# Kernel tuning notes

Measured on AMD Instinct MI355X. Metric: run time of the kernel, lower is better.

The kernel has to match this reference:

```python
import jax, jax.numpy as jnp
import numpy as np

N, E, C, S, G = 20000, 320000, 32, 64, 64
NRAD, HRAD, OUTS, HHEAD, NSH, NL = 8, 64, 16, 64, 9, 2
RCUT = 5.0
LIDX = np.repeat(np.arange(3), [1, 3, 5])  # l index of each of the 9 sh components


def _sph_harm(u):
    # real spherical harmonics up to l=2 on unit vectors, [E,3] -> [E,9]
    x, y, z = u[:, 0], u[:, 1], u[:, 2]
    s3 = jnp.sqrt(jnp.asarray(3.0, u.dtype))
    return jnp.stack([
        jnp.ones_like(x), x, y, z,
        s3 * x * y, s3 * y * z, 0.5 * (3 * z * z - 1.0), s3 * x * z,
        0.5 * s3 * (x * x - y * y)
    ], axis=1)


def _bessel(r):
    # Bessel radial basis with smooth polynomial envelope, [E] -> [E, NRAD]
    n = jnp.arange(1, NRAD + 1, dtype=r.dtype)
    rs = jnp.clip(r, 1e-6, None)[:, None]
    u = jnp.clip(r / RCUT, 0.0, 1.0)
    env = ((1 - u) ** 2 * (1 + 2 * u))[:, None]
    return jnp.sqrt(2.0 / RCUT) * jnp.sin(n * jnp.pi * rs / RCUT) / rs * env


def setup_inputs() -> dict:
    key = jax.random.key(0)
    ks = jax.random.split(key, 16)
    return {
        'vectors': jax.random.normal(ks[0], (E, 3), jnp.float32),
        'node_species': jax.random.randint(ks[1], (N,), 0, S),
        'senders': jax.random.randint(ks[2], (E,), 0, N),
        'receivers': jax.random.randint(ks[3], (E,), 0, N),
        'graph_id': jnp.sort(jax.random.randint(ks[4], (N,), 0, G)),
        'species_embed': jax.random.normal(ks[5], (S, C), jnp.float32) * 0.1,
        'w_r1': jax.random.normal(ks[6], (NRAD, HRAD), jnp.float32) / np.sqrt(NRAD),
        'b_r1': jnp.zeros((HRAD,), jnp.float32),
        'w_r2': jax.random.normal(ks[7], (NL, HRAD, 3 * C), jnp.float32) / np.sqrt(HRAD),
        'w_mix': jax.random.normal(ks[8], (NL, 3, C, C), jnp.float32) / np.sqrt(C),
        'w_sc': jax.random.normal(ks[9], (NL, S, C, C), jnp.float32) / np.sqrt(C),
        'w_readout': jax.random.normal(ks[10], (C, OUTS), jnp.float32) / np.sqrt(C),
        'ln_gamma': jnp.ones((OUTS,), jnp.float32),
        'ln_beta': jnp.zeros((OUTS,), jnp.float32),
        'w_h1': jax.random.normal(ks[11], (OUTS, HHEAD), jnp.float32) / np.sqrt(OUTS),
        'b_h1': jnp.zeros((HHEAD,), jnp.float32),
        'w_h2': jax.random.normal(ks[12], (HHEAD, 1), jnp.float32) / np.sqrt(HHEAD),
        'b_h2': jnp.zeros((1,), jnp.float32),
        'scale': jnp.ones((), jnp.float32),
        'shift': jnp.zeros((), jnp.float32),
    }


def reference(vectors, node_species, senders, receivers, graph_id, species_embed,
              w_r1, b_r1, w_r2, w_mix, w_sc, w_readout, ln_gamma, ln_beta,
              w_h1, b_h1, w_h2, b_h2, scale, shift):
    lidx = jnp.asarray(LIDX)
    # nan-safe edge norms and unit vectors (safe_norm in source)
    r2 = jnp.sum(vectors ** 2, axis=-1)
    r = jnp.where(r2 == 0, 0.0, jnp.sqrt(jnp.where(r2 == 0, 1.0, r2)))
    u = vectors / jnp.where(r == 0, 1.0, r)[:, None]
    sh = _sph_harm(u)                                  # [E,9]
    rad = jax.nn.silu(_bessel(r) @ w_r1 + b_r1)        # [E,HRAD] radial MLP
    h = species_embed[node_species]                    # [N,C] node embedding
    for li in range(NL):
        # per-edge, per-l, per-channel radial weights, expanded to the 9 sh components
        rw = (rad @ w_r2[li]).reshape(E, 3, C)[:, lidx, :]     # [E,9,C]
        # tensor-product message: radial * sender scalars * Y_lm
        msg = sh[:, :, None] * rw * h[senders][:, None, :]     # [E,9,C]
        agg = jax.ops.segment_sum(msg, receivers, num_segments=N)  # [N,9,C]
        # per-irrep (per-l) channel-mixing linear
        mixed = jnp.einsum('nmc,mcd->nmd', agg, w_mix[li][lidx])   # [N,9,C]
        # species-dependent self-connection on the scalar (l=0) channel
        sc = jnp.einsum('nc,ncd->nd', h, w_sc[li][node_species])   # [N,C]
        h = mixed[:, 0, :] + sc + h                                # residual
    readout = h @ w_readout                            # [N,OUTS] (last-block readout)
    mu = jnp.mean(readout, axis=-1, keepdims=True)
    var = jnp.var(readout, axis=-1, keepdims=True)
    nrm = (readout - mu) * jax.lax.rsqrt(var + 1e-6) * ln_gamma + ln_beta
    node_out = (jax.nn.gelu(nrm @ w_h1 + b_h1) @ w_h2 + b_h2)[:, 0]  # [N]
    gsum = jax.ops.segment_sum(node_out, graph_id, num_segments=G)
    cnt = jax.ops.segment_sum(jnp.ones((N,), node_out.dtype), graph_id, num_segments=G)
    gmean = gsum / jnp.clip(cnt, 1.0, None)            # segment-mean node2graph
    return (gmean * scale + shift)[:, None]            # [G,1]
```

## Files before the change

kernel.cpp:

```cpp
#include <hip/hip_runtime.h>
#include <hip/hip_fp16.h>
#include <cstdint>
#include <cmath>

#define NE 320000
#define NN 20000
#define NG 64

typedef __attribute__((ext_vector_type(8))) short s16x8;
typedef __attribute__((ext_vector_type(4))) float f32x4;

static __device__ __forceinline__ unsigned short f32_to_bf16(float x) {
    unsigned int u = __float_as_uint(x);
    u = (u + 0x7fffu + ((u >> 16) & 1u)) >> 16;
    return (unsigned short)u;
}
static __device__ __forceinline__ float bf16_to_f32(unsigned short h) {
    return __uint_as_float(((unsigned int)h) << 16);
}

__global__ __launch_bounds__(256) void setup_kernel(
    const int* __restrict__ spec, const float* __restrict__ emb,
    float* __restrict__ h,
    const float* __restrict__ w_r2,
    unsigned short* __restrict__ wt_hi, unsigned short* __restrict__ wt_lo,
    int* __restrict__ deg, float* __restrict__ gz)
{
    int t = blockIdx.x * 256 + threadIdx.x;
    if (t < NN * 32) h[t] = emb[spec[t >> 5] * 32 + (t & 31)];
    if (t < 4096) {
        int c = t >> 6, k = t & 63;
        float v = w_r2[(c >= 32 ? 6144 : 0) + k * 96 + (c & 31)];
        unsigned short hb = f32_to_bf16(v);
        wt_hi[t] = hb;
        wt_lo[t] = f32_to_bf16(v - bf16_to_f32(hb));
    }
    if (t < NN) deg[t] = 0;
    if (t < 128) gz[t] = 0.0f;
}

__global__ __launch_bounds__(256) void count_kernel(
    const int* __restrict__ recv, int* __restrict__ deg)
{
    int e = blockIdx.x * 256 + threadIdx.x;
    atomicAdd(&deg[recv[e]], 1);
}

__global__ __launch_bounds__(1024) void scan_kernel(
    const int* __restrict__ deg,
    int* __restrict__ rowstart, int* __restrict__ cursor)
{
    __shared__ int tsum[1024];
    const int tid = threadIdx.x;
    const int PER = (NN + 1023) / 1024;
    const int base = tid * PER;

    int s = 0;
    for (int i = 0; i < PER; ++i) {
        int idx = base + i;
        if (idx < NN) s += deg[idx];
    }
    tsum[tid] = s;
    __syncthreads();
    for (int off = 1; off < 1024; off <<= 1) {
        int v = (tid >= off) ? tsum[tid - off] : 0;
        __syncthreads();
        tsum[tid] += v;
        __syncthreads();
    }
    int run = tsum[tid] - s;
    for (int i = 0; i < PER; ++i) {
        int idx = base + i;
        if (idx < NN) {
            rowstart[idx] = run;
            cursor[idx] = run;
            run += deg[idx];
        }
    }
    if (tid == 1023) rowstart[NN] = NE;
}

__global__ __launch_bounds__(256) void scatter_kernel(
    const int* __restrict__ recv, const int* __restrict__ snd,
    int* __restrict__ cursor, int* __restrict__ eperm, int* __restrict__ esnd)
{
    int e = blockIdx.x * 256 + threadIdx.x;
    int slot = atomicAdd(&cursor[recv[e]], 1);
    eperm[e] = slot;
    esnd[slot] = snd[e];
}

__global__ __launch_bounds__(256) void edge_gemm_kernel(
    const float* __restrict__ vectors,
    const float* __restrict__ w_r1,
    const float* __restrict__ b_r1,
    const unsigned short* __restrict__ wt_hi,
    const unsigned short* __restrict__ wt_lo,
    const int* __restrict__ eperm,
    __half* __restrict__ rw0_0,
    __half* __restrict__ rw0_1)
{
    __shared__ __attribute__((aligned(16))) short sh_hi[256 * 72];
    __shared__ __attribute__((aligned(16))) short sh_lo[256 * 72];

    const int tid = threadIdx.x;
    const int e = blockIdx.x * 256 + tid;
    const int slot = eperm[e];

    float x = vectors[3 * e + 0];
    float y = vectors[3 * e + 1];
    float z = vectors[3 * e + 2];
    float r2 = x * x + y * y + z * z;
    float r = (r2 == 0.0f) ? 0.0f : sqrtf(r2);
    float rs = fmaxf(r, 1e-6f);
    float u = fminf(r * 0.2f, 1.0f);
    float env = (1.0f - u) * (1.0f - u) * (1.0f + 2.0f * u);
    float pref = 0.6324555320336759f * env / rs;
    float theta = 0.6283185307179586f * rs;

    float s1 = __sinf(theta), c1 = __cosf(theta);
    float twoc = 2.0f * c1;
    float b[8];
    {
        float sp = 0.0f, s = s1;
#pragma unroll
        for (int n = 0; n < 8; ++n) {
            b[n] = pref * s;
            float nx = twoc * s - sp;
            sp = s; s = nx;
        }
    }

#pragma unroll
    for (int j0 = 0; j0 < 64; j0 += 8) {
        short hibuf[8], lobuf[8];
#pragma unroll
        for (int jj = 0; jj < 8; ++jj) {
            int j = j0 + jj;
            float pre = b_r1[j];
#pragma unroll
            for (int n = 0; n < 8; ++n) pre = fmaf(b[n], w_r1[n * 64 + j], pre);
            float rj = pre * __builtin_amdgcn_rcpf(1.0f + __expf(-pre));
            unsigned short hb = f32_to_bf16(rj);
            float lov = rj - bf16_to_f32(hb);
            hibuf[jj] = (short)hb;
            lobuf[jj] = (short)f32_to_bf16(lov);
        }
        *(s16x8*)&sh_hi[tid * 72 + j0] =
            (s16x8){hibuf[0],hibuf[1],hibuf[2],hibuf[3],hibuf[4],hibuf[5],hibuf[6],hibuf[7]};
        *(s16x8*)&sh_lo[tid * 72 + j0] =
            (s16x8){lobuf[0],lobuf[1],lobuf[2],lobuf[3],lobuf[4],lobuf[5],lobuf[6],lobuf[7]};
    }

    __syncthreads();

    const int wv = tid >> 6;
    const int l = tid & 63;
    const int lrow = l & 15;
    const int lk = l >> 4;

    s16x8 Bhi[4][2], Blo[4][2];
#pragma unroll
    for (int ct = 0; ct < 4; ++ct)
#pragma unroll
        for (int kt = 0; kt < 2; ++kt) {
            int col = ct * 16 + lrow;
            int kof = kt * 32 + lk * 8;
            Bhi[ct][kt] = *(const s16x8*)(wt_hi + col * 64 + kof);
            Blo[ct][kt] = *(const s16x8*)(wt_lo + col * 64 + kof);
        }

    f32x4 acc[4][4];
#pragma unroll
    for (int rt = 0; rt < 4; ++rt)
#pragma unroll
        for (int ct = 0; ct < 4; ++ct) acc[rt][ct] = (f32x4){0.f, 0.f, 0.f, 0.f};

#pragma unroll
    for (int rt = 0; rt < 4; ++rt) {
        int row = wv * 64 + rt * 16 + lrow;
#pragma unroll
        for (int kt = 0; kt < 2; ++kt) {
            s16x8 ahi = *(const s16x8*)&sh_hi[row * 72 + kt * 32 + lk * 8];
            s16x8 alo = *(const s16x8*)&sh_lo[row * 72 + kt * 32 + lk * 8];
#pragma unroll
            for (int ct = 0; ct < 4; ++ct) {
                acc[rt][ct] = __builtin_amdgcn_mfma_f32_16x16x32_bf16(ahi, Bhi[ct][kt], acc[rt][ct], 0, 0, 0);
                acc[rt][ct] = __builtin_amdgcn_mfma_f32_16x16x32_bf16(alo, Bhi[ct][kt], acc[rt][ct], 0, 0, 0);
                acc[rt][ct] = __builtin_amdgcn_mfma_f32_16x16x32_bf16(ahi, Blo[ct][kt], acc[rt][ct], 0, 0, 0);
            }
        }
    }

    __syncthreads();
    __half* stg = (__half*)sh_hi;
#pragma unroll
    for (int rt = 0; rt < 4; ++rt)
#pragma unroll
        for (int ct = 0; ct < 4; ++ct) {
            int col = ct * 16 + lrow;
#pragma unroll
            for (int rr = 0; rr < 4; ++rr) {
                int erow = wv * 64 + rt * 16 + lk * 4 + rr;
                stg[erow * 72 + col] = __float2half_rn(acc[rt][ct][rr]);
            }
        }
    __syncthreads();
    {
        const s16x8* src = (const s16x8*)&sh_hi[tid * 72];
        size_t eb = (size_t)slot * 32;
        s16x8* d0 = (s16x8*)(rw0_0 + eb);
        s16x8* d1 = (s16x8*)(rw0_1 + eb);
        d0[0] = src[0]; d0[1] = src[1]; d0[2] = src[2]; d0[3] = src[3];
        d1[0] = src[4]; d1[1] = src[5]; d1[2] = src[6]; d1[3] = src[7];
    }
}

__device__ __forceinline__ float agg_update_val(
    const __half* __restrict__ rw0h, const float* __restrict__ hin,
    const int* __restrict__ rowstart, const int* __restrict__ esnd,
    const int* __restrict__ spec,
    const float* __restrict__ wmix0, const float* __restrict__ wscl,
    int t, int n, int c, int half)
{
    int s0 = rowstart[n], s1 = rowstart[n + 1];
    float hv = hin[t];

    float p0 = 0.f, p1 = 0.f, p2 = 0.f, p3 = 0.f;
    int k = s0;
    for (; k + 4 <= s1; k += 4) {
        int sA = esnd[k], sB = esnd[k + 1], sC = esnd[k + 2], sD = esnd[k + 3];
        float rA = __half2float(rw0h[(size_t)k * 32 + c]);
        float rB = __half2float(rw0h[(size_t)(k + 1) * 32 + c]);
        float rC = __half2float(rw0h[(size_t)(k + 2) * 32 + c]);
        float rD = __half2float(rw0h[(size_t)(k + 3) * 32 + c]);
        float hA = hin[(size_t)sA * 32 + c];
        float hB = hin[(size_t)sB * 32 + c];
        float hC = hin[(size_t)sC * 32 + c];
        float hD = hin[(size_t)sD * 32 + c];
        p0 = fmaf(rA, hA, p0);
        p1 = fmaf(rB, hB, p1);
        p2 = fmaf(rC, hC, p2);
        p3 = fmaf(rD, hD, p3);
    }
    for (; k < s1; ++k)
        p0 = fmaf(__half2float(rw0h[(size_t)k * 32 + c]),
                  hin[(size_t)esnd[k] * 32 + c], p0);
    float acc = (p0 + p1) + (p2 + p3);

    const float* wsc = wscl + spec[n] * 1024;
    float m0 = 0.f, m1 = 0.f, q0 = 0.f, q1 = 0.f;
#pragma unroll
    for (int cp = 0; cp < 32; cp += 2) {
        float av0 = __shfl(acc, half + cp);
        float hb0 = __shfl(hv, half + cp);
        float av1 = __shfl(acc, half + cp + 1);
        float hb1 = __shfl(hv, half + cp + 1);
        m0 = fmaf(av0, wmix0[cp * 32 + c], m0);
        q0 = fmaf(hb0, wsc[cp * 32 + c], q0);
        m1 = fmaf(av1, wmix0[(cp + 1) * 32 + c], m1);
        q1 = fmaf(hb1, wsc[(cp + 1) * 32 + c], q1);
    }
    return hv + (m0 + m1) + (q0 + q1);
}

__global__ __launch_bounds__(256) void agg_update_kernel(
    const __half* __restrict__ rw0h, const float* __restrict__ hin,
    const int* __restrict__ rowstart, const int* __restrict__ esnd,
    const int* __restrict__ spec,
    const float* __restrict__ wmix0, const float* __restrict__ wscl,
    float* __restrict__ hout)
{
    int t = blockIdx.x * 256 + threadIdx.x;
    int n = t >> 5, c = t & 31;
    int half = (threadIdx.x & 63) & 32;
    hout[t] = agg_update_val(rw0h, hin, rowstart, esnd, spec, wmix0, wscl,
                             t, n, c, half);
}

__global__ __launch_bounds__(256) void agg_readout_kernel(
    const __half* __restrict__ rw0h, const float* __restrict__ hin,
    const int* __restrict__ rowstart, const int* __restrict__ esnd,
    const int* __restrict__ spec,
    const float* __restrict__ wmix0, const float* __restrict__ wscl,
    const int* __restrict__ gid_arr,
    const float* __restrict__ w_ro,
    const float* __restrict__ gamma, const float* __restrict__ beta,
    const float* __restrict__ w_h1, const float* __restrict__ b_h1,
    const float* __restrict__ w_h2, const float* __restrict__ b_h2,
    float* __restrict__ gsum, float* __restrict__ gcnt)
{
    __shared__ int sgid[8];
    __shared__ float sval[8];

    int t = blockIdx.x * 256 + threadIdx.x;
    int n = t >> 5, c = t & 31;
    int half = (threadIdx.x & 63) & 32;

    float outv = agg_update_val(rw0h, hin, rowstart, esnd, spec, wmix0, wscl,
                                t, n, c, half);

    int o = c & 15;
    float r0 = 0.f, r1 = 0.f, r2 = 0.f, r3 = 0.f;
#pragma unroll
    for (int cp = 0; cp < 32; cp += 4) {
        r0 = fmaf(__shfl(outv, half + cp),     w_ro[cp * 16 + o],       r0);
        r1 = fmaf(__shfl(outv, half + cp + 1), w_ro[(cp + 1) * 16 + o], r1);
        r2 = fmaf(__shfl(outv, half + cp + 2), w_ro[(cp + 2) * 16 + o], r2);
        r3 = fmaf(__shfl(outv, half + cp + 3), w_ro[(cp + 3) * 16 + o], r3);
    }
    float ro = (r0 + r1) + (r2 + r3);

    float ssum = ro;
#pragma unroll
    for (int m = 1; m < 16; m <<= 1) ssum += __shfl_xor(ssum, m);
    float mu = ssum * (1.0f / 16.0f);
    float d = ro - mu;
    float vs = d * d;
#pragma unroll
    for (int m = 1; m < 16; m <<= 1) vs += __shfl_xor(vs, m);
    float inv = rsqrtf(vs * (1.0f / 16.0f) + 1e-6f);
    float nrm = d * inv * gamma[o] + beta[o];

    int j1 = c, j2 = c + 32;
    float a1a = b_h1[j1], a1b = 0.f, a2a = b_h1[j2], a2b = 0.f;
#pragma unroll
    for (int oo = 0; oo < 16; oo += 2) {
        float nv0 = __shfl(nrm, half + oo);
        float nv1 = __shfl(nrm, half + oo + 1);
        a1a = fmaf(nv0, w_h1[oo * 64 + j1], a1a);
        a2a = fmaf(nv0, w_h1[oo * 64 + j2], a2a);
        a1b = fmaf(nv1, w_h1[(oo + 1) * 64 + j1], a1b);
        a2b = fmaf(nv1, w_h1[(oo + 1) * 64 + j2], a2b);
    }
    float a1 = a1a + a1b, a2 = a2a + a2b;
    float g1 = 0.5f * a1 * (1.0f + tanhf(0.7978845608028654f * (a1 + 0.044715f * a1 * a1 * a1)));
    float g2 = 0.5f * a2 * (1.0f + tanhf(0.7978845608028654f * (a2 + 0.044715f * a2 * a2 * a2)));
    float partial = fmaf(g1, w_h2[j1], g2 * w_h2[j2]);
#pragma unroll
    for (int m = 1; m < 32; m <<= 1) partial += __shfl_xor(partial, m);

    if (c == 0) {
        int hw = threadIdx.x >> 5;
        sgid[hw] = gid_arr[n];
        sval[hw] = partial + b_h2[0];
    }
    __syncthreads();
    if (threadIdx.x == 0) {
        int g0 = sgid[0];
        float accv = sval[0];
        float cnt = 1.0f;
        for (int i = 1; i < 8; ++i) {
            if (sgid[i] == g0) { accv += sval[i]; cnt += 1.0f; }
            else {
                atomicAdd(&gsum[g0], accv);
                atomicAdd(&gcnt[g0], cnt);
                g0 = sgid[i]; accv = sval[i]; cnt = 1.0f;
            }
        }
        atomicAdd(&gsum[g0], accv);
        atomicAdd(&gcnt[g0], cnt);
    }
}

__global__ void finalize_kernel(const float* __restrict__ gsum,
                                const float* __restrict__ gcnt,
                                const float* __restrict__ scale,
                                const float* __restrict__ shift,
                                float* __restrict__ out)
{
    int g = threadIdx.x;
    if (g < NG) out[g] = gsum[g] / fmaxf(gcnt[g], 1.0f) * scale[0] + shift[0];
}

extern "C" void kernel_launch(void* const* d_in, const int* in_sizes, int n_in,
                              void* d_out, int out_size, void* d_ws, size_t ws_size,
                              hipStream_t stream)
{
    const float* vectors       = (const float*)d_in[0];
    const int*   node_species  = (const int*)d_in[1];
    const int*   senders       = (const int*)d_in[2];
    const int*   receivers     = (const int*)d_in[3];
    const int*   graph_id      = (const int*)d_in[4];
    const float* species_embed = (const float*)d_in[5];
    const float* w_r1          = (const float*)d_in[6];
    const float* b_r1          = (const float*)d_in[7];
    const float* w_r2          = (const float*)d_in[8];
    const float* w_mix         = (const float*)d_in[9];
    const float* w_sc          = (const float*)d_in[10];
    const float* w_ro          = (const float*)d_in[11];
    const float* ln_gamma      = (const float*)d_in[12];
    const float* ln_beta       = (const float*)d_in[13];
    const float* w_h1          = (const float*)d_in[14];
    const float* b_h1          = (const float*)d_in[15];
    const float* w_h2          = (const float*)d_in[16];
    const float* b_h2          = (const float*)d_in[17];
    const float* scale         = (const float*)d_in[18];
    const float* shift         = (const float*)d_in[19];
    float* out = (float*)d_out;

    __half* rw0_0 = (__half*)d_ws;
    __half* rw0_1 = rw0_0 + (size_t)NE * 32;
    float* hA     = (float*)(rw0_1 + (size_t)NE * 32);
    float* hB     = hA + (size_t)NN * 32;
    float* gsum   = hB + (size_t)NN * 32;
    float* gcnt   = gsum + NG;
    unsigned short* wt_hi = (unsigned short*)(gcnt + NG);
    unsigned short* wt_lo = wt_hi + 4096;
    int* deg      = (int*)(wt_lo + 4096);
    int* rowstart = deg + NN;
    int* cursor   = rowstart + NN + 1;
    int* eperm    = cursor + NN + 1;
    int* esnd     = eperm + NE;

    setup_kernel<<<(NN * 32 + 255) / 256, 256, 0, stream>>>(
        node_species, species_embed, hA, w_r2, wt_hi, wt_lo, deg, gsum);

    count_kernel<<<NE / 256, 256, 0, stream>>>(receivers, deg);

    scan_kernel<<<1, 1024, 0, stream>>>(deg, rowstart, cursor);

    scatter_kernel<<<NE / 256, 256, 0, stream>>>(receivers, senders, cursor, eperm, esnd);

    edge_gemm_kernel<<<NE / 256, 256, 0, stream>>>(
        vectors, w_r1, b_r1, wt_hi, wt_lo, eperm, rw0_0, rw0_1);

    agg_update_kernel<<<(NN * 32) / 256, 256, 0, stream>>>(
        rw0_0, hA, rowstart, esnd, node_species, w_mix, w_sc, hB);

    agg_readout_kernel<<<(NN * 32) / 256, 256, 0, stream>>>(
        rw0_1, hB, rowstart, esnd, node_species, w_mix + 3072, w_sc + 65536,
        graph_id, w_ro, ln_gamma, ln_beta, w_h1, b_h1, w_h2, b_h2, gsum, gcnt);

    finalize_kernel<<<1, 64, 0, stream>>>(gsum, gcnt, scale, shift, out);
}
```

Before: 174.7 us.

## Fuse CSR build stages, interleave radial weights, stage sender indices in LDS

```diff
diff --git a/kernel.cpp b/kernel.cpp
--- a/kernel.cpp
+++ b/kernel.cpp
@@ -21,13 +21,13 @@
 
 __global__ __launch_bounds__(256) void setup_kernel(
     const int* __restrict__ spec, const float* __restrict__ emb,
-    float* __restrict__ h,
+    float* __restrict__ hA,
     const float* __restrict__ w_r2,
     unsigned short* __restrict__ wt_hi, unsigned short* __restrict__ wt_lo,
-    int* __restrict__ deg, float* __restrict__ gz)
+    int* __restrict__ deg, float* __restrict__ gz, int* __restrict__ tickets)
 {
     int t = blockIdx.x * 256 + threadIdx.x;
-    if (t < NN * 32) h[t] = emb[spec[t >> 5] * 32 + (t & 31)];
+    if (t < NN * 32) hA[t] = emb[spec[t >> 5] * 32 + (t & 31)];
     if (t < 4096) {
         int c = t >> 6, k = t & 63;
         float v = w_r2[(c >= 32 ? 6144 : 0) + k * 96 + (c & 31)];
@@ -37,24 +37,27 @@
     }
     if (t < NN) deg[t] = 0;
     if (t < 128) gz[t] = 0.0f;
-}
-
-__global__ __launch_bounds__(256) void count_kernel(
-    const int* __restrict__ recv, int* __restrict__ deg)
-{
-    int e = blockIdx.x * 256 + threadIdx.x;
-    atomicAdd(&deg[recv[e]], 1);
-}
-
-__global__ __launch_bounds__(1024) void scan_kernel(
-    const int* __restrict__ deg,
-    int* __restrict__ rowstart, int* __restrict__ cursor)
-{
+    if (t < 2) tickets[t] = 0;
+}
+
+__global__ __launch_bounds__(1024) void count_scan_kernel(
+    const int* __restrict__ recv,
+    int* __restrict__ deg, int* __restrict__ rowstart, int* __restrict__ cursor,
+    int* __restrict__ ticket)
+{
+    __shared__ int is_last;
     __shared__ int tsum[1024];
     const int tid = threadIdx.x;
-    const int PER = (NN + 1023) / 1024;
+    int e = blockIdx.x * 1024 + tid;
+    if (e < NE) atomicAdd(&deg[recv[e]], 1);
+    __threadfence();
+    __syncthreads();
+    if (tid == 0) is_last = (atomicAdd(ticket, 1) == (int)gridDim.x - 1);
+    __syncthreads();
+    if (!is_last) return;
+
+    const int PER = 20;
     const int base = tid * PER;
-
     int s = 0;
     for (int i = 0; i < PER; ++i) {
         int idx = base + i;
@@ -80,32 +83,24 @@
     if (tid == 1023) rowstart[NN] = NE;
 }
 
-__global__ __launch_bounds__(256) void scatter_kernel(
-    const int* __restrict__ recv, const int* __restrict__ snd,
-    int* __restrict__ cursor, int* __restrict__ eperm, int* __restrict__ esnd)
-{
-    int e = blockIdx.x * 256 + threadIdx.x;
-    int slot = atomicAdd(&cursor[recv[e]], 1);
-    eperm[e] = slot;
-    esnd[slot] = snd[e];
-}
-
 __global__ __launch_bounds__(256) void edge_gemm_kernel(
     const float* __restrict__ vectors,
     const float* __restrict__ w_r1,
     const float* __restrict__ b_r1,
     const unsigned short* __restrict__ wt_hi,
     const unsigned short* __restrict__ wt_lo,
-    const int* __restrict__ eperm,
-    __half* __restrict__ rw0_0,
-    __half* __restrict__ rw0_1)
+    const int* __restrict__ recv, const int* __restrict__ snd,
+    int* __restrict__ cursor, int* __restrict__ esnd,
+    __half* __restrict__ rw01)
 {
     __shared__ __attribute__((aligned(16))) short sh_hi[256 * 72];
     __shared__ __attribute__((aligned(16))) short sh_lo[256 * 72];
 
     const int tid = threadIdx.x;
     const int e = blockIdx.x * 256 + tid;
-    const int slot = eperm[e];
+
+    const int slot = atomicAdd(&cursor[recv[e]], 1);
+    esnd[slot] = snd[e];
 
     float x = vectors[3 * e + 0];
     float y = vectors[3 * e + 1];
@@ -208,32 +203,31 @@
     __syncthreads();
     {
         const s16x8* src = (const s16x8*)&sh_hi[tid * 72];
-        size_t eb = (size_t)slot * 32;
-        s16x8* d0 = (s16x8*)(rw0_0 + eb);
-        s16x8* d1 = (s16x8*)(rw0_1 + eb);
-        d0[0] = src[0]; d0[1] = src[1]; d0[2] = src[2]; d0[3] = src[3];
-        d1[0] = src[4]; d1[1] = src[5]; d1[2] = src[6]; d1[3] = src[7];
-    }
-}
-
-__device__ __forceinline__ float agg_update_val(
-    const __half* __restrict__ rw0h, const float* __restrict__ hin,
-    const int* __restrict__ rowstart, const int* __restrict__ esnd,
-    const int* __restrict__ spec,
+        s16x8* d = (s16x8*)(rw01 + (size_t)slot * 64);
+#pragma unroll
+        for (int i = 0; i < 8; ++i) d[i] = src[i];
+    }
+}
+
+__device__ __forceinline__ float agg_core(
+    const __half* __restrict__ rw01, const float* __restrict__ hin,
+    const int* __restrict__ esnd, const int* sesnd, int S0, int lim,
+    int s0, int s1, int loff,
     const float* __restrict__ wmix0, const float* __restrict__ wscl,
-    int t, int n, int c, int half)
-{
-    int s0 = rowstart[n], s1 = rowstart[n + 1];
-    float hv = hin[t];
-
+    int spn, float hv, int c, int half)
+{
     float p0 = 0.f, p1 = 0.f, p2 = 0.f, p3 = 0.f;
     int k = s0;
     for (; k + 4 <= s1; k += 4) {
-        int sA = esnd[k], sB = esnd[k + 1], sC = esnd[k + 2], sD = esnd[k + 3];
-        float rA = __half2float(rw0h[(size_t)k * 32 + c]);
-        float rB = __half2float(rw0h[(size_t)(k + 1) * 32 + c]);
-        float rC = __half2float(rw0h[(size_t)(k + 2) * 32 + c]);
-        float rD = __half2float(rw0h[(size_t)(k + 3) * 32 + c]);
+        int i0 = k - S0;
+        int sA = (i0     < lim) ? sesnd[i0]     : esnd[k];
+        int sB = (i0 + 1 < lim) ? sesnd[i0 + 1] : esnd[k + 1];
+        int sC = (i0 + 2 < lim) ? sesnd[i0 + 2] : esnd[k + 2];
+        int sD = (i0 + 3 < lim) ? sesnd[i0 + 3] : esnd[k + 3];
+        float rA = __half2float(rw01[(size_t)k * 64 + loff + c]);
+        float rB = __half2float(rw01[(size_t)(k + 1) * 64 + loff + c]);
+        float rC = __half2float(rw01[(size_t)(k + 2) * 64 + loff + c]);
+        float rD = __half2float(rw01[(size_t)(k + 3) * 64 + loff + c]);
         float hA = hin[(size_t)sA * 32 + c];
         float hB = hin[(size_t)sB * 32 + c];
         float hC = hin[(size_t)sC * 32 + c];
@@ -243,12 +237,15 @@
         p2 = fmaf(rC, hC, p2);
         p3 = fmaf(rD, hD, p3);
     }
-    for (; k < s1; ++k)
-        p0 = fmaf(__half2float(rw0h[(size_t)k * 32 + c]),
-                  hin[(size_t)esnd[k] * 32 + c], p0);
+    for (; k < s1; ++k) {
+        int i0 = k - S0;
+        int sA = (i0 < lim) ? sesnd[i0] : esnd[k];
+        p0 = fmaf(__half2float(rw01[(size_t)k * 64 + loff + c]),
+                  hin[(size_t)sA * 32 + c], p0);
+    }
     float acc = (p0 + p1) + (p2 + p3);
 
-    const float* wsc = wscl + spec[n] * 1024;
+    const float* wsc = wscl + spn * 1024;
     float m0 = 0.f, m1 = 0.f, q0 = 0.f, q1 = 0.f;
 #pragma unroll
     for (int cp = 0; cp < 32; cp += 2) {
@@ -265,21 +262,32 @@
 }
 
 __global__ __launch_bounds__(256) void agg_update_kernel(
-    const __half* __restrict__ rw0h, const float* __restrict__ hin,
+    const __half* __restrict__ rw01, const float* __restrict__ hin,
     const int* __restrict__ rowstart, const int* __restrict__ esnd,
     const int* __restrict__ spec,
     const float* __restrict__ wmix0, const float* __restrict__ wscl,
     float* __restrict__ hout)
 {
-    int t = blockIdx.x * 256 + threadIdx.x;
+    __shared__ int sesnd[2048];
+    const int tid = threadIdx.x;
+    int t = blockIdx.x * 256 + tid;
     int n = t >> 5, c = t & 31;
-    int half = (threadIdx.x & 63) & 32;
-    hout[t] = agg_update_val(rw0h, hin, rowstart, esnd, spec, wmix0, wscl,
-                             t, n, c, half);
+    int half = (tid & 63) & 32;
+
+    int n0 = blockIdx.x * 8;
+    int S0 = rowstart[n0];
+    int lim = min(rowstart[n0 + 8] - S0, 2048);
+    for (int i = tid; i < lim; i += 256) sesnd[i] = esnd[S0 + i];
+    __syncthreads();
+
+    int s0 = rowstart[n], s1 = rowstart[n + 1];
+    float hv = hin[t];
+    hout[t] = agg_core(rw01, hin, esnd, sesnd, S0, lim, s0, s1, 0,
+                       wmix0, wscl, spec[n], hv, c, half);
 }
 
 __global__ __launch_bounds__(256) void agg_readout_kernel(
-    const __half* __restrict__ rw0h, const float* __restrict__ hin,
+    const __half* __restrict__ rw01, const float* __restrict__ hin,
     const int* __restrict__ rowstart, const int* __restrict__ esnd,
     const int* __restrict__ spec,
     const float* __restrict__ wmix0, const float* __restrict__ wscl,
@@ -288,17 +296,31 @@
     const float* __restrict__ gamma, const float* __restrict__ beta,
     const float* __restrict__ w_h1, const float* __restrict__ b_h1,
     const float* __restrict__ w_h2, const float* __restrict__ b_h2,
-    float* __restrict__ gsum, float* __restrict__ gcnt)
-{
+    float* __restrict__ gsum, float* __restrict__ gcnt,
+    int* __restrict__ ticket,
+    const float* __restrict__ scale, const float* __restrict__ shift,
+    float* __restrict__ out)
+{
+    __shared__ int sesnd[2048];
     __shared__ int sgid[8];
     __shared__ float sval[8];
-
-    int t = blockIdx.x * 256 + threadIdx.x;
+    __shared__ int is_last;
+
+    const int tid = threadIdx.x;
+    int t = blockIdx.x * 256 + tid;
     int n = t >> 5, c = t & 31;
-    int half = (threadIdx.x & 63) & 32;
-
-    float outv = agg_update_val(rw0h, hin, rowstart, esnd, spec, wmix0, wscl,
-                                t, n, c, half);
+    int half = (tid & 63) & 32;
+
+    int n0 = blockIdx.x * 8;
+    int S0 = rowstart[n0];
+    int lim = min(rowstart[n0 + 8] - S0, 2048);
+    for (int i = tid; i < lim; i += 256) sesnd[i] = esnd[S0 + i];
+    __syncthreads();
+
+    int s0 = rowstart[n], s1 = rowstart[n + 1];
+    float hv = hin[t];
+    float outv = agg_core(rw01, hin, esnd, sesnd, S0, lim, s0, s1, 32,
+                          wmix0, wscl, spec[n], hv, c, half);
 
     int o = c & 15;
     float r0 = 0.f, r1 = 0.f, r2 = 0.f, r3 = 0.f;
@@ -334,19 +356,21 @@
         a2b = fmaf(nv1, w_h1[(oo + 1) * 64 + j2], a2b);
     }
     float a1 = a1a + a1b, a2 = a2a + a2b;
-    float g1 = 0.5f * a1 * (1.0f + tanhf(0.7978845608028654f * (a1 + 0.044715f * a1 * a1 * a1)));
-    float g2 = 0.5f * a2 * (1.0f + tanhf(0.7978845608028654f * (a2 + 0.044715f * a2 * a2 * a2)));
+    float g1 = a1 * __builtin_amdgcn_rcpf(
+        1.0f + __expf(-1.5957691216057308f * (a1 + 0.044715f * a1 * a1 * a1)));
+    float g2 = a2 * __builtin_amdgcn_rcpf(
+        1.0f + __expf(-1.5957691216057308f * (a2 + 0.044715f * a2 * a2 * a2)));
     float partial = fmaf(g1, w_h2[j1], g2 * w_h2[j2]);
 #pragma unroll
     for (int m = 1; m < 32; m <<= 1) partial += __shfl_xor(partial, m);
 
     if (c == 0) {
-        int hw = threadIdx.x >> 5;
+        int hw = tid >> 5;
         sgid[hw] = gid_arr[n];
         sval[hw] = partial + b_h2[0];
     }
     __syncthreads();
-    if (threadIdx.x == 0) {
+    if (tid == 0) {
         int g0 = sgid[0];
         float accv = sval[0];
         float cnt = 1.0f;
@@ -361,16 +385,16 @@
         atomicAdd(&gsum[g0], accv);
         atomicAdd(&gcnt[g0], cnt);
     }
-}
-
-__global__ void finalize_kernel(const float* __restrict__ gsum,
-                                const float* __restrict__ gcnt,
-                                const float* __restrict__ scale,
-                                const float* __restrict__ shift,
-                                float* __restrict__ out)
-{
-    int g = threadIdx.x;
-    if (g < NG) out[g] = gsum[g] / fmaxf(gcnt[g], 1.0f) * scale[0] + shift[0];
+
+    __threadfence();
+    __syncthreads();
+    if (tid == 0) is_last = (atomicAdd(ticket, 1) == (int)gridDim.x - 1);
+    __syncthreads();
+    if (is_last && tid < NG) {
+        float gs = atomicAdd(&gsum[tid], 0.0f);
+        float gc = atomicAdd(&gcnt[tid], 0.0f);
+        out[tid] = gs / fmaxf(gc, 1.0f) * scale[0] + shift[0];
+    }
 }
 
 extern "C" void kernel_launch(void* const* d_in, const int* in_sizes, int n_in,
@@ -399,9 +423,8 @@
     const float* shift         = (const float*)d_in[19];
     float* out = (float*)d_out;
 
-    __half* rw0_0 = (__half*)d_ws;
-    __half* rw0_1 = rw0_0 + (size_t)NE * 32;
-    float* hA     = (float*)(rw0_1 + (size_t)NE * 32);
+    __half* rw01  = (__half*)d_ws;
+    float* hA     = (float*)(rw01 + (size_t)NE * 64);
     float* hB     = hA + (size_t)NN * 32;
     float* gsum   = hB + (size_t)NN * 32;
     float* gcnt   = gsum + NG;
@@ -410,27 +433,23 @@
     int* deg      = (int*)(wt_lo + 4096);
     int* rowstart = deg + NN;
     int* cursor   = rowstart + NN + 1;
-    int* eperm    = cursor + NN + 1;
-    int* esnd     = eperm + NE;
+    int* esnd     = cursor + NN + 1;
+    int* tickets  = esnd + NE;
 
     setup_kernel<<<(NN * 32 + 255) / 256, 256, 0, stream>>>(
-        node_species, species_embed, hA, w_r2, wt_hi, wt_lo, deg, gsum);
-
-    count_kernel<<<NE / 256, 256, 0, stream>>>(receivers, deg);
-
-    scan_kernel<<<1, 1024, 0, stream>>>(deg, rowstart, cursor);
-
-    scatter_kernel<<<NE / 256, 256, 0, stream>>>(receivers, senders, cursor, eperm, esnd);
+        node_species, species_embed, hA, w_r2, wt_hi, wt_lo, deg, gsum, tickets);
+
+    count_scan_kernel<<<(NE + 1023) / 1024, 1024, 0, stream>>>(
+        receivers, deg, rowstart, cursor, tickets);
 
     edge_gemm_kernel<<<NE / 256, 256, 0, stream>>>(
-        vectors, w_r1, b_r1, wt_hi, wt_lo, eperm, rw0_0, rw0_1);
+        vectors, w_r1, b_r1, wt_hi, wt_lo, receivers, senders, cursor, esnd, rw01);
 
     agg_update_kernel<<<(NN * 32) / 256, 256, 0, stream>>>(
-        rw0_0, hA, rowstart, esnd, node_species, w_mix, w_sc, hB);
+        rw01, hA, rowstart, esnd, node_species, w_mix, w_sc, hB);
 
     agg_readout_kernel<<<(NN * 32) / 256, 256, 0, stream>>>(
-        rw0_1, hB, rowstart, esnd, node_species, w_mix + 3072, w_sc + 65536,
-        graph_id, w_ro, ln_gamma, ln_beta, w_h1, b_h1, w_h2, b_h2, gsum, gcnt);
-
-    finalize_kernel<<<1, 64, 0, stream>>>(gsum, gcnt, scale, shift, out);
-}
+        rw01, hB, rowstart, esnd, node_species, w_mix + 3072, w_sc + 65536,
+        graph_id, w_ro, ln_gamma, ln_beta, w_h1, b_h1, w_h2, b_h2,
+        gsum, gcnt, tickets + 1, scale, shift, out);
+}
```

Result: slower. 381.7 us (+118.5%).
